# Kernel optimization log

Hardware: AMD Instinct MI355X
Metric: run time of the kernel (lower is better)

Reference implementation:

```python
import jax, jax.numpy as jnp
import numpy as np

N_NODES = 16384
N_EDGES = 524288
N_GRAPHS = 64
HID = 128
FILT = 128
NG = 51
NL = 6
NODE_CLASS = 119
CUTOFF = 10.0
LOG2 = float(np.log(2.0))


def ssp(x):
    # ShiftedSoftplus
    return jax.nn.softplus(x) - LOG2


def setup_inputs() -> dict:
    key = jax.random.key(0)
    ks = jax.random.split(key, 20)
    z = jax.random.randint(ks[0], (N_NODES,), 0, NODE_CLASS)
    # uniform in a cube of side 5 -> all pairwise dists < cutoff=10
    pos = jax.random.uniform(ks[1], (N_NODES, 3), dtype=jnp.float32) * 5.0
    batch = jnp.sort(jax.random.randint(ks[2], (N_NODES,), 0, N_GRAPHS))
    edge_index = jax.random.randint(ks[3], (2, N_EDGES), 0, N_NODES)
    def lin(k, fan_in, shape):
        return jax.random.normal(k, shape, dtype=jnp.float32) / np.sqrt(fan_in)
    params = {
        'emb_table': jax.random.normal(ks[4], (NODE_CLASS, HID), dtype=jnp.float32),
        # per-interaction stacked weights, layout [in, out]
        'mlp1_w': lin(ks[5], NG, (NL, NG, FILT)),
        'mlp1_b': jnp.zeros((NL, FILT), jnp.float32),
        'mlp2_w': lin(ks[6], FILT, (NL, FILT, FILT)),
        'mlp2_b': jnp.zeros((NL, FILT), jnp.float32),
        'cl1_w': lin(ks[7], HID, (NL, HID, FILT)),   # CFConv.lin1, no bias
        'cl2_w': lin(ks[8], FILT, (NL, FILT, HID)),
        'cl2_b': jnp.zeros((NL, HID), jnp.float32),
        'lin_w': lin(ks[9], HID, (NL, HID, HID)),
        'lin_b': jnp.zeros((NL, HID), jnp.float32),
        'out1_w': lin(ks[10], HID, (HID, HID)),
        'out1_b': jnp.zeros((HID,), jnp.float32),
        'out2_w': lin(ks[11], HID, (HID, HID)),
        'out2_b': jnp.zeros((HID,), jnp.float32),
    }
    return dict(z=z, pos=pos, batch=batch, edge_index=edge_index, **params)


def reference(z, pos, batch, edge_index, emb_table, mlp1_w, mlp1_b, mlp2_w,
              mlp2_b, cl1_w, cl2_w, cl2_b, lin_w, lin_b, out1_w, out1_b,
              out2_w, out2_b):
    row, col = edge_index[0], edge_index[1]
    h = emb_table[z]                                   # [N, HID]
    # edge distances
    diff = pos[row] - pos[col]                         # [E, 3]
    edge_weight = jnp.sqrt(jnp.sum(diff * diff, axis=-1))  # [E]
    # GaussianSmearing
    offset = jnp.linspace(0.0, CUTOFF, NG, dtype=jnp.float32)
    coeff = -0.5 / (offset[1] - offset[0]) ** 2
    d = edge_weight[:, None] - offset[None, :]
    edge_attr = jnp.exp(coeff * d * d)                 # [E, NG]
    # cosine cutoff
    C = 0.5 * (jnp.cos(edge_weight * jnp.pi / CUTOFF) + 1.0)  # [E]
    for i in range(NL):
        # filter network on edge attrs
        W = ssp(edge_attr @ mlp1_w[i] + mlp1_b[i]) @ mlp2_w[i] + mlp2_b[i]
        W = W * C[:, None]                             # [E, FILT]
        xh = h @ cl1_w[i]                              # [N, FILT]
        msg = xh[col] * W                              # gather + modulate
        agg = jax.ops.segment_sum(msg, row, num_segments=N_NODES)
        out = agg @ cl2_w[i] + cl2_b[i]
        out = ssp(out)
        out = out @ lin_w[i] + lin_b[i]
        h = h + out
    h = ssp(h @ out1_w + out1_b) @ out2_w + out2_b     # [N, HID]
    # scatter-mean pooling over graphs
    sums = jax.ops.segment_sum(h, batch, num_segments=N_GRAPHS)
    counts = jax.ops.segment_sum(jnp.ones((N_NODES,), h.dtype), batch,
                                 num_segments=N_GRAPHS)
    return sums / jnp.maximum(counts, 1.0)[:, None]    # [G, HID]
```

## Files before the change

### kernel.cpp

```cpp
#include <hip/hip_runtime.h>
#include <hip/hip_fp16.h>
#include <math.h>

#define N_NODES 16384
#define N_EDGES 524288
#define N_GRAPHS 64
#define HID 128
#define FILT 128
#define NG 51
#define NL 6
#define TROWS 2048
#define DMAX 8.66025404f
#define DSTEP (DMAX / (TROWS - 1))
#define INV_DSTEP ((TROWS - 1) / DMAX)
#define EU 3
#define TSTRIDE 132
#define TP 136

typedef _Float16 half8 __attribute__((ext_vector_type(8)));
typedef float f32x4 __attribute__((ext_vector_type(4)));

__device__ __forceinline__ float ssp(float x) {
    float sp = (x > 20.0f) ? x : log1pf(__expf(x));
    return sp - 0.6931471805599453f;
}

__global__ void k_embed(const int* __restrict__ z, const float* __restrict__ emb,
                        float* __restrict__ h) {
    int i = blockIdx.x * blockDim.x + threadIdx.x;
    int n = i >> 7, c = i & 127;
    h[i] = emb[z[n] * HID + c];
}

__global__ void k_hist(const int* __restrict__ ei, int* __restrict__ cnt) {
    int e = blockIdx.x * blockDim.x + threadIdx.x;
    if (e < N_EDGES) atomicAdd(&cnt[ei[e]], 1);
}

__global__ __launch_bounds__(1024) void k_scan(const int* __restrict__ cnt,
                                               int* __restrict__ rowptr,
                                               int* __restrict__ wo) {
    __shared__ int sums[1024];
    int t = threadIdx.x;
    int loc[16];
    int s = 0;
    #pragma unroll
    for (int i = 0; i < 16; ++i) { loc[i] = cnt[t * 16 + i]; s += loc[i]; }
    sums[t] = s;
    __syncthreads();
    for (int off = 1; off < 1024; off <<= 1) {
        int v = sums[t];
        int u = (t >= off) ? sums[t - off] : 0;
        __syncthreads();
        sums[t] = v + u;
        __syncthreads();
    }
    int ex = sums[t] - s;
    #pragma unroll
    for (int i = 0; i < 16; ++i) {
        rowptr[t * 16 + i] = ex;
        wo[t * 16 + i] = ex;
        ex += loc[i];
    }
    if (t == 1023) rowptr[16384] = ex;
}

__global__ void k_scatter(const int* __restrict__ ei, const float* __restrict__ pos,
                          int* __restrict__ wo, int2* __restrict__ meta) {
    int e = blockIdx.x * blockDim.x + threadIdx.x;
    if (e >= N_EDGES) return;
    int r = ei[e], c = ei[N_EDGES + e];
    int p = atomicAdd(&wo[r], 1);
    float dx = pos[r * 3 + 0] - pos[c * 3 + 0];
    float dy = pos[r * 3 + 1] - pos[c * 3 + 1];
    float dz = pos[r * 3 + 2] - pos[c * 3 + 2];
    float ew = sqrtf(dx * dx + dy * dy + dz * dz);
    meta[p] = make_int2(c, __float_as_int(ew));
}

__global__ void k_wpack(const float* __restrict__ src, __half* __restrict__ dst,
                        int nmat) {
    int idx = blockIdx.x * 256 + threadIdx.x;
    if (idx >= nmat * 2048) return;
    int mat = idx >> 11;
    int r = idx & 2047;
    int kk = r >> 9, n = (r >> 6) & 7, lane = r & 63;
    const float* S = src + (size_t)mat * 16384;
    __half* D = dst + (size_t)mat * 16384 + (size_t)r * 8;
    int k0 = kk * 32 + (lane >> 4) * 8;
    int c = n * 16 + (lane & 15);
    #pragma unroll
    for (int j = 0; j < 8; ++j)
        D[j] = __float2half_rn(S[(k0 + j) * 128 + c]);
}

__global__ __launch_bounds__(256, 4) void k_tab2(
    const float* __restrict__ mlp1_w, const float* __restrict__ mlp1_b,
    const float* __restrict__ mlp2_w, const float* __restrict__ mlp2_b,
    __half* __restrict__ ftab)
{
    __shared__ float tls[4 * 4 * TSTRIDE];
    const int w = threadIdx.x >> 6;
    const int lane = threadIdx.x & 63;
    const int gr = blockIdx.x * 16 + w * 4;
    const int layer = gr >> 11;
    const int r0 = gr & (TROWS - 1);
    const float* W1 = mlp1_w + (size_t)layer * NG * FILT;
    const float* B1 = mlp1_b + (size_t)layer * FILT;
    const float* W2 = mlp2_w + (size_t)layer * FILT * FILT;
    const float* B2 = mlp2_b + (size_t)layer * FILT;
    float* tp = &tls[w * 4 * TSTRIDE];
    float acc1[4][2];
    {
        float ba = B1[lane], bb = B1[lane + 64];
        #pragma unroll
        for (int j = 0; j < 4; ++j) { acc1[j][0] = ba; acc1[j][1] = bb; }
    }
    for (int k = 0; k < NG; ++k) {
        float wa = W1[k * FILT + lane];
        float wb = W1[k * FILT + lane + 64];
        #pragma unroll
        for (int j = 0; j < 4; ++j) {
            float dd = (float)(r0 + j) * DSTEP - 0.2f * (float)k;
            float g = __expf(-12.5f * dd * dd);
            acc1[j][0] = fmaf(g, wa, acc1[j][0]);
            acc1[j][1] = fmaf(g, wb, acc1[j][1]);
        }
    }
    #pragma unroll
    for (int j = 0; j < 4; ++j) {
        tp[j * TSTRIDE + lane] = ssp(acc1[j][0]);
        tp[j * TSTRIDE + lane + 64] = ssp(acc1[j][1]);
    }
    __syncthreads();
    float acc2[4][2];
    {
        float ba = B2[lane], bb = B2[lane + 64];
        #pragma unroll
        for (int j = 0; j < 4; ++j) { acc2[j][0] = ba; acc2[j][1] = bb; }
    }
    #pragma unroll 4
    for (int k = 0; k < FILT; k += 2) {
        float w0a = W2[k * FILT + lane];
        float w0b = W2[k * FILT + lane + 64];
        float w1a = W2[(k + 1) * FILT + lane];
        float w1b = W2[(k + 1) * FILT + lane + 64];
        #pragma unroll
        for (int j = 0; j < 4; ++j) {
            float2 t = *(float2*)&tp[j * TSTRIDE + k];
            acc2[j][0] = fmaf(t.x, w0a, fmaf(t.y, w1a, acc2[j][0]));
            acc2[j][1] = fmaf(t.x, w0b, fmaf(t.y, w1b, acc2[j][1]));
        }
    }
    #pragma unroll
    for (int j = 0; j < 4; ++j) {
        float d = (float)(r0 + j) * DSTEP;
        float C = 0.5f * (__cosf(d * 0.31415926535f) + 1.0f);
        __half* out = ftab + (size_t)layer * TROWS * FILT + (size_t)(r0 + j) * FILT;
        out[lane] = __float2half_rn(acc2[j][0] * C);
        out[lane + 64] = __float2half_rn(acc2[j][1] * C);
    }
}

__global__ __launch_bounds__(256, 7) void k_edge9(
    const int2* __restrict__ meta, const int* __restrict__ rowptr,
    const __half* __restrict__ xh, const __half* __restrict__ tab,
    __half* __restrict__ agg)
{
    const int row = blockIdx.x * 4 + (threadIdx.x >> 6);
    const int lane = threadIdx.x & 63;
    const int half = lane >> 5;
    const int c4 = (lane & 31) * 4;
    const int es = rowptr[row], ee = rowptr[row + 1];
    float4 acc = make_float4(0.f, 0.f, 0.f, 0.f);
    if (es < ee) {
        int2 mcur[EU];
        #pragma unroll
        for (int u = 0; u < EU; ++u)
            mcur[u] = meta[min(es + 2 * u + half, ee - 1)];
        for (int e = es; e < ee; e += 2 * EU) {
            const int en = e + 2 * EU;
            int2 mnext[EU];
            if (en < ee) {
                #pragma unroll
                for (int u = 0; u < EU; ++u)
                    mnext[u] = meta[min(en + 2 * u + half, ee - 1)];
            }
            float2 t0h[EU], t1h[EU], xr[EU];
            float f[EU], sc[EU];
            #pragma unroll
            for (int u = 0; u < EU; ++u) {
                sc[u] = (e + 2 * u + half < ee) ? 1.f : 0.f;
                float d = __int_as_float(mcur[u].y);
                float uu = d * INV_DSTEP;
                int i0 = min((int)uu, TROWS - 2);
                f[u] = uu - (float)i0;
                t0h[u] = *(const float2*)&tab[(size_t)i0 * FILT + c4];
                t1h[u] = *(const float2*)&tab[(size_t)(i0 + 1) * FILT + c4];
                xr[u]  = *(const float2*)&xh[(size_t)mcur[u].x * FILT + c4];
            }
            #pragma unroll
            for (int u = 0; u < EU; ++u) {
                float2 T0a = __half22float2(*reinterpret_cast<__half2*>(&t0h[u].x));
                float2 T0b = __half22float2(*reinterpret_cast<__half2*>(&t0h[u].y));
                float2 T1a = __half22float2(*reinterpret_cast<__half2*>(&t1h[u].x));
                float2 T1b = __half22float2(*reinterpret_cast<__half2*>(&t1h[u].y));
                float2 x01 = __half22float2(*reinterpret_cast<__half2*>(&xr[u].x));
                float2 x23 = __half22float2(*reinterpret_cast<__half2*>(&xr[u].y));
                acc.x = fmaf(fmaf(f[u], T1a.x - T0a.x, T0a.x) * sc[u], x01.x, acc.x);
                acc.y = fmaf(fmaf(f[u], T1a.y - T0a.y, T0a.y) * sc[u], x01.y, acc.y);
                acc.z = fmaf(fmaf(f[u], T1b.x - T0b.x, T0b.x) * sc[u], x23.x, acc.z);
                acc.w = fmaf(fmaf(f[u], T1b.y - T0b.y, T0b.y) * sc[u], x23.y, acc.w);
            }
            #pragma unroll
            for (int u = 0; u < EU; ++u) mcur[u] = mnext[u];
        }
        acc.x += __shfl_xor(acc.x, 32, 64);
        acc.y += __shfl_xor(acc.y, 32, 64);
        acc.z += __shfl_xor(acc.z, 32, 64);
        acc.w += __shfl_xor(acc.w, 32, 64);
    }
    if (half == 0) {
        float2 st;
        ((__half2*)&st)[0] = __floats2half2_rn(acc.x, acc.y);
        ((__half2*)&st)[1] = __floats2half2_rn(acc.z, acc.w);
        *(float2*)&agg[(size_t)row * FILT + c4] = st;
    }
}

template<bool A32, bool RESID, bool G3>
__global__ __launch_bounds__(256, 8) void k_nodeM2(
    const __half* __restrict__ Ah, const float* __restrict__ Af,
    const __half* __restrict__ Wp1, const float* __restrict__ B1,
    const __half* __restrict__ Wp2, const float* __restrict__ B2,
    const float* __restrict__ Hin, float* __restrict__ Hout,
    const __half* __restrict__ Wp3, __half* __restrict__ XHout)
{
    __shared__ __half tp[16 * TP];
    const int w = threadIdx.x >> 6;
    const int lane = threadIdx.x & 63;
    const int lm = lane & 15;
    const int lk = lane >> 4;
    const int rbase = blockIdx.x * 16;
    const int n0 = w * 2;

    f32x4 acc[2];
    #pragma unroll
    for (int t = 0; t < 2; ++t) acc[t] = (f32x4){0.f, 0.f, 0.f, 0.f};
    #pragma unroll
    for (int kk = 0; kk < 4; ++kk) {
        half8 a;
        if (A32) {
            const float* ap = &Af[(size_t)(rbase + lm) * 128 + kk * 32 + lk * 8];
            float4 v0 = *(const float4*)ap;
            float4 v1 = *(const float4*)(ap + 4);
            a[0] = (_Float16)v0.x; a[1] = (_Float16)v0.y;
            a[2] = (_Float16)v0.z; a[3] = (_Float16)v0.w;
            a[4] = (_Float16)v1.x; a[5] = (_Float16)v1.y;
            a[6] = (_Float16)v1.z; a[7] = (_Float16)v1.w;
        } else {
            a = *(const half8*)&Ah[(size_t)(rbase + lm) * 128 + kk * 32 + lk * 8];
        }
        #pragma unroll
        for (int t = 0; t < 2; ++t) {
            half8 b = *(const half8*)&Wp1[((kk * 8 + n0 + t) * 64 + lane) * 8];
            acc[t] = __builtin_amdgcn_mfma_f32_16x16x32_f16(a, b, acc[t], 0, 0, 0);
        }
    }
    #pragma unroll
    for (int t = 0; t < 2; ++t) {
        int n = n0 + t;
        float bv = B1[n * 16 + lm];
        #pragma unroll
        for (int q = 0; q < 4; ++q)
            tp[(lk * 4 + q) * TP + n * 16 + lm] = __float2half_rn(ssp(acc[t][q] + bv));
    }
    __syncthreads();
    f32x4 acc2[2];
    #pragma unroll
    for (int t = 0; t < 2; ++t) acc2[t] = (f32x4){0.f, 0.f, 0.f, 0.f};
    #pragma unroll
    for (int kk = 0; kk < 4; ++kk) {
        half8 a = *(const half8*)&tp[lm * TP + kk * 32 + lk * 8];
        #pragma unroll
        for (int t = 0; t < 2; ++t) {
            half8 b = *(const half8*)&Wp2[((kk * 8 + n0 + t) * 64 + lane) * 8];
            acc2[t] = __builtin_amdgcn_mfma_f32_16x16x32_f16(a, b, acc2[t], 0, 0, 0);
        }
    }
    __syncthreads();
    #pragma unroll
    for (int t = 0; t < 2; ++t) {
        int n = n0 + t;
        float bv = B2[n * 16 + lm];
        #pragma unroll
        for (int q = 0; q < 4; ++q) {
            size_t ro = (size_t)(rbase + lk * 4 + q) * 128 + n * 16 + lm;
            float v = acc2[t][q] + bv;
            if (RESID) v += Hin[ro];
            Hout[ro] = v;
            if (G3) tp[(lk * 4 + q) * TP + n * 16 + lm] = __float2half_rn(v);
        }
    }
    if (G3) {
        __syncthreads();
        f32x4 acc3[2];
        #pragma unroll
        for (int t = 0; t < 2; ++t) acc3[t] = (f32x4){0.f, 0.f, 0.f, 0.f};
        #pragma unroll
        for (int kk = 0; kk < 4; ++kk) {
            half8 a = *(const half8*)&tp[lm * TP + kk * 32 + lk * 8];
            #pragma unroll
            for (int t = 0; t < 2; ++t) {
                half8 b = *(const half8*)&Wp3[((kk * 8 + n0 + t) * 64 + lane) * 8];
                acc3[t] = __builtin_amdgcn_mfma_f32_16x16x32_f16(a, b, acc3[t], 0, 0, 0);
            }
        }
        __syncthreads();
        #pragma unroll
        for (int t = 0; t < 2; ++t) {
            int n = n0 + t;
            #pragma unroll
            for (int q = 0; q < 4; ++q)
                tp[(lk * 4 + q) * TP + n * 16 + lm] = __float2half_rn(acc3[t][q]);
        }
        __syncthreads();
        int idx = threadIdx.x;
        int row = idx >> 4, k8 = (idx & 15) * 8;
        *(float4*)&XHout[(size_t)(rbase + row) * 128 + k8] =
            *(float4*)&tp[row * TP + k8];
    }
}

__global__ __launch_bounds__(256, 8) void k_gemm0M2(
    const float* __restrict__ Af, const __half* __restrict__ Wp,
    __half* __restrict__ Y)
{
    __shared__ __half tp[16 * TP];
    const int w = threadIdx.x >> 6;
    const int lane = threadIdx.x & 63;
    const int lm = lane & 15;
    const int lk = lane >> 4;
    const int rbase = blockIdx.x * 16;
    const int n0 = w * 2;
    f32x4 acc[2];
    #pragma unroll
    for (int t = 0; t < 2; ++t) acc[t] = (f32x4){0.f, 0.f, 0.f, 0.f};
    #pragma unroll
    for (int kk = 0; kk < 4; ++kk) {
        const float* ap = &Af[(size_t)(rbase + lm) * 128 + kk * 32 + lk * 8];
        float4 v0 = *(const float4*)ap;
        float4 v1 = *(const float4*)(ap + 4);
        half8 a;
        a[0] = (_Float16)v0.x; a[1] = (_Float16)v0.y;
        a[2] = (_Float16)v0.z; a[3] = (_Float16)v0.w;
        a[4] = (_Float16)v1.x; a[5] = (_Float16)v1.y;
        a[6] = (_Float16)v1.z; a[7] = (_Float16)v1.w;
        #pragma unroll
        for (int t = 0; t < 2; ++t) {
            half8 b = *(const half8*)&Wp[((kk * 8 + n0 + t) * 64 + lane) * 8];
            acc[t] = __builtin_amdgcn_mfma_f32_16x16x32_f16(a, b, acc[t], 0, 0, 0);
        }
    }
    #pragma unroll
    for (int t = 0; t < 2; ++t) {
        int n = n0 + t;
        #pragma unroll
        for (int q = 0; q < 4; ++q)
            tp[(lk * 4 + q) * TP + n * 16 + lm] = __float2half_rn(acc[t][q]);
    }
    __syncthreads();
    int idx = threadIdx.x;
    int row = idx >> 4, k8 = (idx & 15) * 8;
    *(float4*)&Y[(size_t)(rbase + row) * 128 + k8] = *(float4*)&tp[row * TP + k8];
}

__global__ __launch_bounds__(128) void k_pool2(const float* __restrict__ x,
                                               const int* __restrict__ batch,
                                               float* __restrict__ gsum) {
    const int c = threadIdx.x;
    const int n0 = blockIdx.x * 64;
    float acc = 0.f;
    int cur = batch[n0];
    for (int i = 0; i < 64; ++i) {
        int g = batch[n0 + i];
        float v = x[(size_t)(n0 + i) * 128 + c];
        if (g != cur) {
            atomicAdd(&gsum[cur * 128 + c], acc);
            acc = 0.f;
            cur = g;
        }
        acc += v;
    }
    atomicAdd(&gsum[cur * 128 + c], acc);
}

__global__ void k_div(const float* __restrict__ gsum, const int* __restrict__ batch,
                      float* __restrict__ out) {
    int g = blockIdx.x;
    int c = threadIdx.x;
    int a = 0, b = N_NODES;
    while (a < b) { int m = (a + b) >> 1; if (batch[m] < g) a = m + 1; else b = m; }
    int lo = a;
    b = N_NODES;
    while (a < b) { int m = (a + b) >> 1; if (batch[m] < g + 1) a = m + 1; else b = m; }
    int cnt = a - lo;
    out[g * 128 + c] = gsum[g * 128 + c] / fmaxf((float)cnt, 1.0f);
}

extern "C" void kernel_launch(void* const* d_in, const int* in_sizes, int n_in,
                              void* d_out, int out_size, void* d_ws, size_t ws_size,
                              hipStream_t stream) {
    const int*   z       = (const int*)  d_in[0];
    const float* pos     = (const float*)d_in[1];
    const int*   batch   = (const int*)  d_in[2];
    const int*   ei      = (const int*)  d_in[3];
    const float* emb     = (const float*)d_in[4];
    const float* mlp1_w  = (const float*)d_in[5];
    const float* mlp1_b  = (const float*)d_in[6];
    const float* mlp2_w  = (const float*)d_in[7];
    const float* mlp2_b  = (const float*)d_in[8];
    const float* cl1_w   = (const float*)d_in[9];
    const float* cl2_w   = (const float*)d_in[10];
    const float* cl2_b   = (const float*)d_in[11];
    const float* lin_w   = (const float*)d_in[12];
    const float* lin_b   = (const float*)d_in[13];
    const float* out1_w  = (const float*)d_in[14];
    const float* out1_b  = (const float*)d_in[15];
    const float* out2_w  = (const float*)d_in[16];
    const float* out2_b  = (const float*)d_in[17];

    float* ws     = (float*)d_ws;
    float* h      = ws;
    float* aggf   = h + (size_t)N_NODES * HID;
    __half* agg16 = (__half*)aggf;
    __half* xh16  = (__half*)(aggf + (size_t)N_NODES * HID);
    float* nxt    = aggf + (size_t)N_NODES * HID + (size_t)N_NODES * HID / 2;
    int2*  meta   = (int2*)nxt;
    int*   cnt    = (int*)(meta + N_EDGES);
    int*   rowptr = cnt + N_NODES;
    int*   wo     = rowptr + N_NODES + 1;
    float* gsum   = (float*)(wo + N_NODES);
    __half* ftab  = (__half*)(gsum + N_GRAPHS * 128);
    __half* wpk   = ftab + (size_t)NL * TROWS * FILT;

    hipMemsetAsync(cnt, 0, N_NODES * sizeof(int), stream);
    hipMemsetAsync(gsum, 0, N_GRAPHS * 128 * sizeof(float), stream);
    k_embed<<<N_NODES * HID / 256, 256, 0, stream>>>(z, emb, h);
    k_hist<<<N_EDGES / 256, 256, 0, stream>>>(ei, cnt);
    k_scan<<<1, 1024, 0, stream>>>(cnt, rowptr, wo);
    k_scatter<<<N_EDGES / 256, 256, 0, stream>>>(ei, pos, wo, meta);
    k_tab2<<<NL * TROWS / 16, 256, 0, stream>>>(mlp1_w, mlp1_b, mlp2_w, mlp2_b, ftab);
    k_wpack<<<(6 * 2048 + 255) / 256, 256, 0, stream>>>(cl1_w, wpk, 6);
    k_wpack<<<(6 * 2048 + 255) / 256, 256, 0, stream>>>(cl2_w, wpk + (size_t)6 * 16384, 6);
    k_wpack<<<(6 * 2048 + 255) / 256, 256, 0, stream>>>(lin_w, wpk + (size_t)12 * 16384, 6);
    k_wpack<<<(2048 + 255) / 256, 256, 0, stream>>>(out1_w, wpk + (size_t)18 * 16384, 1);
    k_wpack<<<(2048 + 255) / 256, 256, 0, stream>>>(out2_w, wpk + (size_t)19 * 16384, 1);

    k_gemm0M2<<<N_NODES / 16, 256, 0, stream>>>(h, wpk, xh16);
    for (int i = 0; i < NL; ++i) {
        k_edge9<<<N_NODES / 4, 256, 0, stream>>>(
            meta, rowptr, xh16, ftab + (size_t)i * TROWS * FILT, agg16);
        if (i < NL - 1) {
            k_nodeM2<false, true, true><<<N_NODES / 16, 256, 0, stream>>>(
                agg16, nullptr,
                wpk + (size_t)(6 + i) * 16384, cl2_b + (size_t)i * HID,
                wpk + (size_t)(12 + i) * 16384, lin_b + (size_t)i * HID,
                h, h, wpk + (size_t)(i + 1) * 16384, xh16);
        } else {
            k_nodeM2<false, true, false><<<N_NODES / 16, 256, 0, stream>>>(
                agg16, nullptr,
                wpk + (size_t)(6 + i) * 16384, cl2_b + (size_t)i * HID,
                wpk + (size_t)(12 + i) * 16384, lin_b + (size_t)i * HID,
                h, h, nullptr, nullptr);
        }
    }
    k_nodeM2<true, false, false><<<N_NODES / 16, 256, 0, stream>>>(
        nullptr, h, wpk + (size_t)18 * 16384, out1_b,
        wpk + (size_t)19 * 16384, out2_b, nullptr, aggf, nullptr, nullptr);
    k_pool2<<<N_NODES / 64, 128, 0, stream>>>(aggf, batch, gsum);
    k_div<<<N_GRAPHS, 128, 0, stream>>>(gsum, batch, (float*)d_out);
}
```

Measured before the change: 466.1 us.

## Widen edge gather to 16-byte loads with four edges per wave, fp16 math

The edge aggregation kernel now has each lane load 8 fp16 channels (16-byte vector loads) and processes four edges in parallel per wave, two unrolled, instead of 4 channels over two edges with three unrolled. The filter interpolation is done in fp16 before accumulating in fp32, and the cross-quarter reduction uses two shuffles. The explicit software prefetch of the next edge metadata is dropped. This aims to cut the number of memory instructions per gathered byte, at the cost of reduced precision in the interpolation and less latency hiding from the removed prefetch.

```diff
diff --git a/kernel.cpp b/kernel.cpp
--- a/kernel.cpp
+++ b/kernel.cpp
@@ -13,7 +13,7 @@
 #define DMAX 8.66025404f
 #define DSTEP (DMAX / (TROWS - 1))
 #define INV_DSTEP ((TROWS - 1) / DMAX)
-#define EU 3
+#define EU2 2
 #define TSTRIDE 132
 #define TP 136
 
@@ -162,69 +162,62 @@
     }
 }
 
-__global__ __launch_bounds__(256, 7) void k_edge9(
+__global__ __launch_bounds__(256, 7) void k_edge10(
     const int2* __restrict__ meta, const int* __restrict__ rowptr,
     const __half* __restrict__ xh, const __half* __restrict__ tab,
     __half* __restrict__ agg)
 {
     const int row = blockIdx.x * 4 + (threadIdx.x >> 6);
     const int lane = threadIdx.x & 63;
-    const int half = lane >> 5;
-    const int c4 = (lane & 31) * 4;
+    const int q = lane >> 4;
+    const int ch8 = (lane & 15) * 8;
     const int es = rowptr[row], ee = rowptr[row + 1];
-    float4 acc = make_float4(0.f, 0.f, 0.f, 0.f);
+    float acc[8];
+    #pragma unroll
+    for (int j = 0; j < 8; ++j) acc[j] = 0.f;
     if (es < ee) {
-        int2 mcur[EU];
-        #pragma unroll
-        for (int u = 0; u < EU; ++u)
-            mcur[u] = meta[min(es + 2 * u + half, ee - 1)];
-        for (int e = es; e < ee; e += 2 * EU) {
-            const int en = e + 2 * EU;
-            int2 mnext[EU];
-            if (en < ee) {
-                #pragma unroll
-                for (int u = 0; u < EU; ++u)
-                    mnext[u] = meta[min(en + 2 * u + half, ee - 1)];
-            }
-            float2 t0h[EU], t1h[EU], xr[EU];
-            float f[EU], sc[EU];
+        for (int e = es; e < ee; e += 4 * EU2) {
+            int2 m[EU2];
             #pragma unroll
-            for (int u = 0; u < EU; ++u) {
-                sc[u] = (e + 2 * u + half < ee) ? 1.f : 0.f;
-                float d = __int_as_float(mcur[u].y);
+            for (int u = 0; u < EU2; ++u)
+                m[u] = meta[min(e + 4 * u + q, ee - 1)];
+            half8 t0[EU2], t1[EU2], xv[EU2];
+            float f[EU2], sc[EU2];
+            #pragma unroll
+            for (int u = 0; u < EU2; ++u) {
+                sc[u] = (e + 4 * u + q < ee) ? 1.f : 0.f;
+                float d = __int_as_float(m[u].y);
                 float uu = d * INV_DSTEP;
                 int i0 = min((int)uu, TROWS - 2);
                 f[u] = uu - (float)i0;
-                t0h[u] = *(const float2*)&tab[(size_t)i0 * FILT + c4];
-                t1h[u] = *(const float2*)&tab[(size_t)(i0 + 1) * FILT + c4];
-                xr[u]  = *(const float2*)&xh[(size_t)mcur[u].x * FILT + c4];
+                t0[u] = *(const half8*)&tab[(size_t)i0 * FILT + ch8];
+                t1[u] = *(const half8*)&tab[(size_t)(i0 + 1) * FILT + ch8];
+                xv[u] = *(const half8*)&xh[(size_t)m[u].x * FILT + ch8];
             }
             #pragma unroll
-            for (int u = 0; u < EU; ++u) {
-                float2 T0a = __half22float2(*reinterpret_cast<__half2*>(&t0h[u].x));
-                float2 T0b = __half22float2(*reinterpret_cast<__half2*>(&t0h[u].y));
-                float2 T1a = __half22float2(*reinterpret_cast<__half2*>(&t1h[u].x));
-                float2 T1b = __half22float2(*reinterpret_cast<__half2*>(&t1h[u].y));
-                float2 x01 = __half22float2(*reinterpret_cast<__half2*>(&xr[u].x));
-                float2 x23 = __half22float2(*reinterpret_cast<__half2*>(&xr[u].y));
-                acc.x = fmaf(fmaf(f[u], T1a.x - T0a.x, T0a.x) * sc[u], x01.x, acc.x);
-                acc.y = fmaf(fmaf(f[u], T1a.y - T0a.y, T0a.y) * sc[u], x01.y, acc.y);
-                acc.z = fmaf(fmaf(f[u], T1b.x - T0b.x, T0b.x) * sc[u], x23.x, acc.z);
-                acc.w = fmaf(fmaf(f[u], T1b.y - T0b.y, T0b.y) * sc[u], x23.y, acc.w);
+            for (int u = 0; u < EU2; ++u) {
+                _Float16 fh = (_Float16)f[u];
+                _Float16 sh = (_Float16)sc[u];
+                #pragma unroll
+                for (int j = 0; j < 8; ++j) {
+                    _Float16 w = (_Float16)((t0[u][j] + fh * (t1[u][j] - t0[u][j])) * sh);
+                    acc[j] += (float)w * (float)xv[u][j];
+                }
             }
-            #pragma unroll
-            for (int u = 0; u < EU; ++u) mcur[u] = mnext[u];
-        }
-        acc.x += __shfl_xor(acc.x, 32, 64);
-        acc.y += __shfl_xor(acc.y, 32, 64);
-        acc.z += __shfl_xor(acc.z, 32, 64);
-        acc.w += __shfl_xor(acc.w, 32, 64);
-    }
-    if (half == 0) {
-        float2 st;
-        ((__half2*)&st)[0] = __floats2half2_rn(acc.x, acc.y);
-        ((__half2*)&st)[1] = __floats2half2_rn(acc.z, acc.w);
-        *(float2*)&agg[(size_t)row * FILT + c4] = st;
+        }
+        #pragma unroll
+        for (int j = 0; j < 8; ++j) {
+            acc[j] += __shfl_xor(acc[j], 16, 64);
+            acc[j] += __shfl_xor(acc[j], 32, 64);
+        }
+    }
+    if (q == 0) {
+        float4 v;
+        ((__half2*)&v)[0] = __floats2half2_rn(acc[0], acc[1]);
+        ((__half2*)&v)[1] = __floats2half2_rn(acc[2], acc[3]);
+        ((__half2*)&v)[2] = __floats2half2_rn(acc[4], acc[5]);
+        ((__half2*)&v)[3] = __floats2half2_rn(acc[6], acc[7]);
+        *(float4*)&agg[(size_t)row * FILT + ch8] = v;
     }
 }
 
@@ -326,9 +319,9 @@
         }
         __syncthreads();
         int idx = threadIdx.x;
-        int row = idx >> 4, k8 = (idx & 15) * 8;
-        *(float4*)&XHout[(size_t)(rbase + row) * 128 + k8] =
-            *(float4*)&tp[row * TP + k8];
+        int r2 = idx >> 4, k8 = (idx & 15) * 8;
+        *(float4*)&XHout[(size_t)(rbase + r2) * 128 + k8] =
+            *(float4*)&tp[r2 * TP + k8];
     }
 }
 
@@ -371,8 +364,8 @@
     }
     __syncthreads();
     int idx = threadIdx.x;
-    int row = idx >> 4, k8 = (idx & 15) * 8;
-    *(float4*)&Y[(size_t)(rbase + row) * 128 + k8] = *(float4*)&tp[row * TP + k8];
+    int r2 = idx >> 4, k8 = (idx & 15) * 8;
+    *(float4*)&Y[(size_t)(rbase + r2) * 128 + k8] = *(float4*)&tp[r2 * TP + k8];
 }
 
 __global__ __launch_bounds__(128) void k_pool2(const float* __restrict__ x,
@@ -459,7 +452,7 @@
 
     k_gemm0M2<<<N_NODES / 16, 256, 0, stream>>>(h, wpk, xh16);
     for (int i = 0; i < NL; ++i) {
-        k_edge9<<<N_NODES / 4, 256, 0, stream>>>(
+        k_edge10<<<N_NODES / 4, 256, 0, stream>>>(
             meta, rowptr, xh16, ftab + (size_t)i * TROWS * FILT, agg16);
         if (i < NL - 1) {
             k_nodeM2<false, true, true><<<N_NODES / 16, 256, 0, stream>>>(
```

Result: faster. 398.5 us (-14.5%).
